# Performance work log

Measured on AMD Instinct MI355X. Metric: run time of the kernel, lower is better.

Reference implementation:

```python
import jax, jax.numpy as jnp
import numpy as np

B, N, C = 4, 16384, 512
HEADS = 16
HEADC = C // HEADS
HIDDEN = int(C * 4.0)


def setup_inputs() -> dict:
    key = jax.random.key(0)
    ks = jax.random.split(key, 8)
    s1 = 1.0 / np.sqrt(C)
    s2 = 1.0 / np.sqrt(HIDDEN)
    return {
        "x": jax.random.normal(ks[0], (B, N, C), jnp.float32),
        "mask_matrix": jnp.zeros((1,), jnp.int32),
        "norm1_w": jnp.ones((C,), jnp.float32),
        "norm1_b": jnp.zeros((C,), jnp.float32),
        "kln_w": jnp.ones((HEADS, 1, HEADC), jnp.float32),
        "kln_b": jnp.zeros((HEADS, 1, HEADC), jnp.float32),
        "vln_w": jnp.ones((HEADS, 1, HEADC), jnp.float32),
        "vln_b": jnp.zeros((HEADS, 1, HEADC), jnp.float32),
        "norm2_w": jnp.ones((C,), jnp.float32),
        "norm2_b": jnp.zeros((C,), jnp.float32),
        "fc1_w": jax.random.uniform(ks[1], (HIDDEN, C), jnp.float32, -s1, s1),
        "fc1_b": jax.random.uniform(ks[2], (HIDDEN,), jnp.float32, -s1, s1),
        "fc2_w": jax.random.uniform(ks[3], (C, HIDDEN), jnp.float32, -s2, s2),
        "fc2_b": jax.random.uniform(ks[4], (C,), jnp.float32, -s2, s2),
    }


def _ln(t, w, b, eps=1e-5):
    # standard nn.LayerNorm: biased variance, eps inside sqrt
    mean = t.mean(-1, keepdims=True)
    var = ((t - mean) ** 2).mean(-1, keepdims=True)
    return w * (t - mean) / jnp.sqrt(var + eps) + b


def _ln_std(t, w, b, eps=1e-5):
    # custom LayerNorm: unbiased std (torch.std), eps added to std
    d = t.shape[-1]
    mean = t.mean(-1, keepdims=True)
    var = ((t - mean) ** 2).sum(-1, keepdims=True) / (d - 1)
    return w * ((t - mean) / (jnp.sqrt(var) + eps)) + b


def reference(x, mask_matrix, norm1_w, norm1_b, kln_w, kln_b, vln_w, vln_b,
              norm2_w, norm2_b, fc1_w, fc1_b, fc2_w, fc2_b):
    b, n, c = x.shape
    shortcut = x
    h = _ln(x, norm1_w, norm1_b)
    # simple_attn (softmax-free linear attention)
    qkv = h.reshape(b, n, HEADS, HEADC).transpose(0, 2, 1, 3)  # [B,H,N,D]
    q = qkv
    k = _ln_std(qkv, kln_w, kln_b)
    v = _ln_std(qkv, vln_w, vln_b)
    kv = jnp.einsum('bhnd,bhne->bhde', k, v) / n        # [B,H,D,D]
    attn = jnp.einsum('bhnd,bhde->bhne', q, kv)          # [B,H,N,D]
    attn = attn.transpose(0, 2, 1, 3).reshape(b, n, c)
    h = attn + h                                          # residual inside simple_attn (bias = x post-norm1)
    x = shortcut + h
    # MLP branch
    m = _ln(x, norm2_w, norm2_b)
    m = jax.nn.gelu(m @ fc1_w.T + fc1_b, approximate=False)
    m = m @ fc2_w.T + fc2_b
    return x + m
```

## Files before the change

kernel.cpp:

```cpp
#include <hip/hip_runtime.h>
#include <cstdint>

#define BB 4
#define NN 16384
#define CC 512
#define HH 16
#define DD 32
#define HID 2048
#define MTOT (BB * NN)

typedef __bf16 bf16_t;
typedef __bf16 bf16x8 __attribute__((ext_vector_type(8)));
typedef __bf16 bf16x4 __attribute__((ext_vector_type(4)));
typedef float  f32x4  __attribute__((ext_vector_type(4)));
typedef float  f32x16 __attribute__((ext_vector_type(16)));

__device__ __forceinline__ void gload_lds16(const void* g, void* l) {
  auto gp = reinterpret_cast<const __attribute__((address_space(1))) char*>(
      reinterpret_cast<uintptr_t>(g));
  auto lp = reinterpret_cast<__attribute__((address_space(3))) char*>(
      reinterpret_cast<uintptr_t>(l));
  __builtin_amdgcn_global_load_lds(gp, lp, 16, 0, 0);
}

__global__ __launch_bounds__(256) void cvt_bf16_kernel(const float* __restrict__ src,
                                                       bf16_t* __restrict__ dst) {
  const long i = ((long)blockIdx.x * 256 + threadIdx.x) * 4;
  const f32x4 v = *(const f32x4*)(src + i);
  bf16x4 o;
  o[0] = (bf16_t)v[0]; o[1] = (bf16_t)v[1]; o[2] = (bf16_t)v[2]; o[3] = (bf16_t)v[3];
  *(bf16x4*)(dst + i) = o;
}

__global__ __launch_bounds__(256) void norm1_kernel(const float* __restrict__ x,
                                                    const float* __restrict__ w,
                                                    const float* __restrict__ bvec,
                                                    bf16_t* __restrict__ h) {
  const int wv = threadIdx.x >> 6, l = threadIdx.x & 63;
  const long tok = (long)blockIdx.x * 4 + wv;
  const int c0 = l * 8;
  const f32x4 a = *(const f32x4*)(x + tok * CC + c0);
  const f32x4 b = *(const f32x4*)(x + tok * CC + c0 + 4);
  float v[8];
#pragma unroll
  for (int i = 0; i < 4; ++i) { v[i] = a[i]; v[4 + i] = b[i]; }
  float s = 0.f, s2 = 0.f;
#pragma unroll
  for (int i = 0; i < 8; ++i) { s += v[i]; s2 += v[i] * v[i]; }
  for (int off = 32; off; off >>= 1) { s += __shfl_xor(s, off); s2 += __shfl_xor(s2, off); }
  const float mean = s * (1.f / CC);
  const float var  = fmaxf(s2 * (1.f / CC) - mean * mean, 0.f);
  const float rstd = rsqrtf(var + 1e-5f);
  const f32x4 w0 = *(const f32x4*)(w + c0), w1 = *(const f32x4*)(w + c0 + 4);
  const f32x4 b0 = *(const f32x4*)(bvec + c0), b1 = *(const f32x4*)(bvec + c0 + 4);
  bf16x8 o;
#pragma unroll
  for (int i = 0; i < 4; ++i) {
    o[i]     = (bf16_t)(w0[i] * (v[i] - mean) * rstd + b0[i]);
    o[4 + i] = (bf16_t)(w1[i] * (v[4 + i] - mean) * rstd + b1[i]);
  }
  *(bf16x8*)(h + tok * CC + c0) = o;
}

__global__ __launch_bounds__(256) void kv_partial_kernel(const bf16_t* __restrict__ h,
                                                         const float* __restrict__ klw,
                                                         const float* __restrict__ klb,
                                                         const float* __restrict__ vlw,
                                                         const float* __restrict__ vlb,
                                                         float* __restrict__ kvp) {
  __shared__ bf16_t kb[256 * 32];
  __shared__ bf16_t vb[256 * 32];
  __shared__ float scratch[192 * 16];
  const int tid = threadIdx.x;
  const int bh = blockIdx.x >> 6, chunk = blockIdx.x & 63;
  const int head = bh & 15;
  const int b = bh >> 4;
  const long tok0 = ((long)b << 14) + chunk * 256;
  const bf16_t* src = h + (tok0 + tid) * (long)CC + head * DD;
  float hv[32];
  {
    float s = 0.f, s2 = 0.f;
#pragma unroll
    for (int c = 0; c < 4; ++c) {
      const bf16x8 r = *(const bf16x8*)(src + c * 8);
#pragma unroll
      for (int j = 0; j < 8; ++j) {
        hv[c * 8 + j] = (float)r[j]; s += hv[c * 8 + j]; s2 += hv[c * 8 + j] * hv[c * 8 + j];
      }
    }
    const float mean = s * (1.f / 32.f);
    const float varu = fmaxf((s2 - 32.f * mean * mean) * (1.f / 31.f), 0.f);
    const float inv = 1.f / (sqrtf(varu) + 1e-5f);
    const int sx = (tid >> 1) & 3;
#pragma unroll
    for (int c = 0; c < 4; ++c) {
      bf16x8 kc, vc;
#pragma unroll
      for (int j = 0; j < 8; ++j) {
        const int d = c * 8 + j;
        const float t = (hv[d] - mean) * inv;
        kc[j] = (bf16_t)(klw[head * DD + d] * t + klb[head * DD + d]);
        vc[j] = (bf16_t)(vlw[head * DD + d] * t + vlb[head * DD + d]);
      }
      *(bf16x8*)((char*)kb + tid * 64 + ((c ^ sx) * 16)) = kc;
      *(bf16x8*)((char*)vb + tid * 64 + ((c ^ sx) * 16)) = vc;
    }
  }
  __syncthreads();
  const int g = tid >> 6, l = tid & 63;
  const int d0 = (l >> 3) * 4, e0 = (l & 7) * 4;
  const int ck = (l >> 3) >> 1, hk = (l >> 3) & 1;
  const int ce = (l & 7) >> 1, he = l & 1;
  float a[4][4] = {};
  for (int t = g; t < 256; t += 4) {
    const int tx = (t >> 1) & 3;
    const bf16x4 kq = *(const bf16x4*)((const char*)kb + t * 64 + ((ck ^ tx) * 16) + hk * 8);
    const bf16x4 vq = *(const bf16x4*)((const char*)vb + t * 64 + ((ce ^ tx) * 16) + he * 8);
    float kf[4], vf[4];
#pragma unroll
    for (int i2 = 0; i2 < 4; ++i2) { kf[i2] = (float)kq[i2]; vf[i2] = (float)vq[i2]; }
#pragma unroll
    for (int i2 = 0; i2 < 4; ++i2)
#pragma unroll
      for (int j2 = 0; j2 < 4; ++j2) a[i2][j2] += kf[i2] * vf[j2];
  }
  __syncthreads();
  if (g) {
#pragma unroll
    for (int i2 = 0; i2 < 4; ++i2)
#pragma unroll
      for (int j2 = 0; j2 < 4; ++j2)
        scratch[((g - 1) * 64 + l) * 16 + i2 * 4 + j2] = a[i2][j2];
  }
  __syncthreads();
  if (!g) {
#pragma unroll
    for (int gg = 0; gg < 3; ++gg)
#pragma unroll
      for (int i2 = 0; i2 < 4; ++i2)
#pragma unroll
        for (int j2 = 0; j2 < 4; ++j2)
          a[i2][j2] += scratch[(gg * 64 + l) * 16 + i2 * 4 + j2];
    float* dst = kvp + ((long)(bh * 64 + chunk) << 10);
#pragma unroll
    for (int i2 = 0; i2 < 4; ++i2) {
      f32x4 st;
      st[0] = a[i2][0]; st[1] = a[i2][1]; st[2] = a[i2][2]; st[3] = a[i2][3];
      *(f32x4*)&dst[(d0 + i2) * 32 + e0] = st;
    }
  }
}

__global__ __launch_bounds__(256) void kv_reduce_kernel(const float* __restrict__ kvp,
                                                        bf16_t* __restrict__ kvT) {
  const int bh = blockIdx.x;
  const int i4 = threadIdx.x * 4;
  const int d = i4 >> 5, e0 = i4 & 31;
  float s[4] = {};
  const float* p = kvp + ((long)bh << 16) + i4;
  for (int ch = 0; ch < 64; ++ch) {
    const f32x4 t = *(const f32x4*)(p + (ch << 10));
    s[0] += t[0]; s[1] += t[1]; s[2] += t[2]; s[3] += t[3];
  }
  const float sc = 1.f / (float)NN;
  bf16_t* q = kvT + ((long)bh << 10);
#pragma unroll
  for (int j = 0; j < 4; ++j) q[(e0 + j) * 32 + d] = (bf16_t)(s[j] * sc);
}

#define ASTRIDE 520
__global__ __launch_bounds__(256) void attn_fused_kernel(const float* __restrict__ x,
                                                         const bf16_t* __restrict__ h,
                                                         const bf16_t* __restrict__ kvTg,
                                                         const float* __restrict__ n2w,
                                                         const float* __restrict__ n2b,
                                                         bf16_t* __restrict__ x2b,
                                                         bf16_t* __restrict__ mout) {
  __shared__ bf16_t attn_s[32 * ASTRIDE];
  const int tid = threadIdx.x;
  const int wv = tid >> 6, lane = tid & 63;
  const int lr = lane & 15, kg = lane >> 4;
  const long tok0 = (long)blockIdx.x * 32;
  const int b = (int)(tok0 >> 14);
  const bf16_t* kvsrc = kvTg + ((long)b << 14);

  {
    const int tt = wv & 1, hh = wv >> 1;
    const bf16_t* arow = h + (tok0 + tt * 16 + lr) * (long)CC + kg * 8;
    const f32x4 zero = {};
#pragma unroll
    for (int hi = 0; hi < 8; ++hi) {
      const int hd = hh * 8 + hi;
      const bf16_t* kvh = kvsrc + (hd << 10) + kg * 8;
      const bf16x8 af = *(const bf16x8*)(arow + hd * DD);
      const bf16x8 b0 = *(const bf16x8*)(kvh + lr * 32);
      const bf16x8 b1 = *(const bf16x8*)(kvh + (16 + lr) * 32);
      const f32x4 a0 = __builtin_amdgcn_mfma_f32_16x16x32_bf16(af, b0, zero, 0, 0, 0);
      const f32x4 a1 = __builtin_amdgcn_mfma_f32_16x16x32_bf16(af, b1, zero, 0, 0, 0);
      const int rbase = tt * 16 + kg * 4;
#pragma unroll
      for (int rg = 0; rg < 4; ++rg) {
        attn_s[(rbase + rg) * ASTRIDE + hd * 32 + lr]      = (bf16_t)a0[rg];
        attn_s[(rbase + rg) * ASTRIDE + hd * 32 + 16 + lr] = (bf16_t)a1[rg];
      }
    }
  }

  const int c0 = lane * 8;
  const f32x4 w0 = *(const f32x4*)(n2w + c0), w1 = *(const f32x4*)(n2w + c0 + 4);
  const f32x4 bb0 = *(const f32x4*)(n2b + c0), bb1 = *(const f32x4*)(n2b + c0 + 4);

  const long tokp = tok0 + wv * 8;
  f32x4 xa = *(const f32x4*)(x + tokp * CC + c0);
  f32x4 xb = *(const f32x4*)(x + tokp * CC + c0 + 4);
  bf16x8 hv = *(const bf16x8*)(h + tokp * CC + c0);
  __syncthreads();

#pragma unroll
  for (int it = 0; it < 8; ++it) {
    const int tl = wv * 8 + it;
    const long tok = tok0 + tl;
    f32x4 xa1, xb1;
    bf16x8 hv1;
    if (it < 7) {
      xa1 = *(const f32x4*)(x + (tok + 1) * CC + c0);
      xb1 = *(const f32x4*)(x + (tok + 1) * CC + c0 + 4);
      hv1 = *(const bf16x8*)(h + (tok + 1) * CC + c0);
    }
    const bf16x8 av = *(const bf16x8*)&attn_s[tl * ASTRIDE + c0];
    float x2[8];
#pragma unroll
    for (int i = 0; i < 4; ++i) {
      x2[i]     = xa[i] + (float)hv[i]     + (float)av[i];
      x2[4 + i] = xb[i] + (float)hv[4 + i] + (float)av[4 + i];
    }
    float s = 0.f, s2 = 0.f;
#pragma unroll
    for (int i = 0; i < 8; ++i) { s += x2[i]; s2 += x2[i] * x2[i]; }
    for (int off = 32; off; off >>= 1) { s += __shfl_xor(s, off); s2 += __shfl_xor(s2, off); }
    const float mean = s * (1.f / CC);
    const float var  = fmaxf(s2 * (1.f / CC) - mean * mean, 0.f);
    const float rstd = rsqrtf(var + 1e-5f);
    bf16x8 ox, om;
#pragma unroll
    for (int i = 0; i < 4; ++i) {
      ox[i]     = (bf16_t)x2[i];
      ox[4 + i] = (bf16_t)x2[4 + i];
      om[i]     = (bf16_t)(w0[i] * (x2[i] - mean) * rstd + bb0[i]);
      om[4 + i] = (bf16_t)(w1[i] * (x2[4 + i] - mean) * rstd + bb1[i]);
    }
    *(bf16x8*)(x2b + tok * CC + c0) = ox;
    *(bf16x8*)(mout + tok * CC + c0) = om;
    xa = xa1; xb = xb1; hv = hv1;
  }
}

template <int K, int NOUT, int BN, bool GELU>
__global__ __launch_bounds__(512, 2) void gemm8p_kernel(const bf16_t* __restrict__ A,
                                                        const bf16_t* __restrict__ Bw,
                                                        const float* __restrict__ bias,
                                                        bf16_t* __restrict__ outb,
                                                        float* __restrict__ outf,
                                                        const bf16_t* __restrict__ x2b) {
  constexpr int NTILE = NOUT / BN;
  constexpr int NT = K / 64;
  constexpr int NI = NT / 2;
  constexpr int WNSPAN = BN / 4;
  constexpr int NF2 = WNSPAN / 32;
  constexpr int BLOADS = BN / 128;
  constexpr int ABYT = 32768;
  constexpr int BBYT = BN * 128;
  constexpr int BUFB = ABYT + BBYT;
  constexpr int KSB = BN * 64;

  __shared__ char lds[2 * BUFB];

  const int tid = threadIdx.x;
  const int wid = tid >> 6, lane = tid & 63;
  const int wm = wid >> 2, wn = wid & 3;
  const int l31 = lane & 31, kg5 = lane >> 5;

  int bid = blockIdx.x;
  const int qq = gridDim.x >> 3;
  bid = (bid & 7) * qq + (bid >> 3);
  const long row0 = (long)(bid / NTILE) * 256;
  const long col0 = (long)(bid % NTILE) * BN;

  const int srow = tid >> 2;
  const int ssw = (((srow >> 1) & 3) ^ ((srow >> 3) & 3));
  const int sce = (((tid & 3) ^ ssw) << 3);
  const bf16_t* pA = A + (row0 + srow) * (long)K + sce;
  const bf16_t* pB = Bw + (col0 + srow) * (long)K + sce;
  char* ldsp = (char*)lds;

  auto SA = [&](int buf, int ks, int kt) {
    char* d_ = ldsp + buf * BUFB + ks * 16384 + tid * 16;
    const bf16_t* g_ = pA + (long)kt * 64 + ks * 32;
    gload_lds16(g_, d_);
    gload_lds16(g_ + 128L * K, d_ + 8192);
  };
  auto SB = [&](int buf, int ks, int kt) {
    char* d_ = ldsp + buf * BUFB + ABYT + ks * KSB + tid * 16;
    const bf16_t* g_ = pB + (long)kt * 64 + ks * 32;
    gload_lds16(g_, d_);
    if constexpr (BLOADS == 2) gload_lds16(g_ + 128L * K, d_ + 8192);
  };

  f32x16 acc[4][NF2] = {};
  bf16x8 af[4], bf[NF2];

  const int swz = ((l31 >> 1) & 3) ^ ((l31 >> 3) & 3);
  const int cb0 = (((0 << 1) | kg5) ^ swz) << 4;
  const int cb1 = (((1 << 1) | kg5) ^ swz) << 4;
  const char* aR = ldsp + (wm * 128 + l31) * 64;
  const char* bR = ldsp + ABYT + (wn * WNSPAN + l31) * 64;

  auto RD = [&](int buf, int ks, int k16) {
    const int cb = k16 ? cb1 : cb0;
    const char* a_ = aR + buf * BUFB + ks * 16384 + cb;
    const char* b_ = bR + buf * BUFB + ks * KSB + cb;
#pragma unroll
    for (int mf = 0; mf < 4; ++mf) af[mf] = *(const bf16x8*)(a_ + mf * 2048);
#pragma unroll
    for (int nf = 0; nf < NF2; ++nf) bf[nf] = *(const bf16x8*)(b_ + nf * 2048);
  };
  auto MM = [&]() {
    __builtin_amdgcn_s_setprio(1);
#pragma unroll
    for (int mf = 0; mf < 4; ++mf)
#pragma unroll
      for (int nf = 0; nf < NF2; ++nf)
        acc[mf][nf] =
            __builtin_amdgcn_mfma_f32_32x32x16_bf16(af[mf], bf[nf], acc[mf][nf], 0, 0, 0);
    __builtin_amdgcn_s_setprio(0);
  };
  auto W2U = [&]() {
    if constexpr (BLOADS == 2) asm volatile("s_waitcnt vmcnt(8)" ::: "memory");
    else                       asm volatile("s_waitcnt vmcnt(6)" ::: "memory");
  };
  auto W1U = [&]() {
    if constexpr (BLOADS == 2) asm volatile("s_waitcnt vmcnt(4)" ::: "memory");
    else                       asm volatile("s_waitcnt vmcnt(3)" ::: "memory");
  };
#define BARX() __builtin_amdgcn_s_barrier()
#define LGKM0() asm volatile("s_waitcnt lgkmcnt(0)" ::: "memory")
#define W0U() asm volatile("s_waitcnt vmcnt(0)" ::: "memory")

  SA(0, 0, 0); SB(0, 0, 0);
  SA(0, 1, 0); SB(0, 1, 0);
  SA(1, 0, 1); SB(1, 0, 1);
  W2U();
  BARX();

  for (int i = 0; i < NI; ++i) {
    const int t1 = 2 * i + 1, tA = 2 * i + 2, tB = 2 * i + 3;
    RD(0, 0, 0); SA(1, 1, t1);
    BARX(); LGKM0(); MM(); BARX();
    RD(0, 0, 1); SB(1, 1, t1);
    BARX(); LGKM0(); MM(); W2U(); BARX();
    RD(0, 1, 0); if (tA < NT) SA(0, 0, tA);
    BARX(); LGKM0(); MM(); BARX();
    RD(0, 1, 1); if (tA < NT) SB(0, 0, tA);
    BARX(); LGKM0(); MM();
    if (tA < NT) W2U(); else W1U();
    BARX();
    RD(1, 0, 0); if (tA < NT) SA(0, 1, tA);
    BARX(); LGKM0(); MM(); BARX();
    RD(1, 0, 1); if (tA < NT) SB(0, 1, tA);
    BARX(); LGKM0(); MM();
    if (tA < NT) W2U(); else W0U();
    BARX();
    RD(1, 1, 0); if (tB < NT) SA(1, 0, tB);
    BARX(); LGKM0(); MM(); BARX();
    RD(1, 1, 1); if (tB < NT) SB(1, 0, tB);
    BARX(); LGKM0(); MM();
    if (tB < NT) W2U();
    BARX();
  }
#undef BARX
#undef LGKM0
#undef W0U

#pragma unroll
  for (int mf = 0; mf < 4; ++mf) {
#pragma unroll
    for (int nf = 0; nf < NF2; ++nf) {
      const long col = col0 + wn * WNSPAN + nf * 32 + l31;
      const float bs = bias[col];
#pragma unroll
      for (int r = 0; r < 16; ++r) {
        const long row = row0 + wm * 128 + mf * 32 + (r & 3) + 8 * (r >> 2) + 4 * kg5;
        const float v = acc[mf][nf][r] + bs;
        if constexpr (GELU) {
          const float u = 0.7978845608028654f * (v + 0.044715f * v * v * v);
          const float gv = v / (1.f + __expf(-2.f * u));
          outb[row * NOUT + col] = (bf16_t)gv;
        } else {
          outf[row * NOUT + col] = (float)x2b[row * NOUT + col] + v;
        }
      }
    }
  }
}

extern "C" void kernel_launch(void* const* d_in, const int* in_sizes, int n_in,
                              void* d_out, int out_size, void* d_ws, size_t ws_size,
                              hipStream_t stream) {
  const float* x   = (const float*)d_in[0];
  const float* n1w = (const float*)d_in[2];
  const float* n1b = (const float*)d_in[3];
  const float* klw = (const float*)d_in[4];
  const float* klb = (const float*)d_in[5];
  const float* vlw = (const float*)d_in[6];
  const float* vlb = (const float*)d_in[7];
  const float* n2w = (const float*)d_in[8];
  const float* n2b = (const float*)d_in[9];
  const float* w1f = (const float*)d_in[10];
  const float* b1  = (const float*)d_in[11];
  const float* w2f = (const float*)d_in[12];
  const float* b2  = (const float*)d_in[13];
  float* out = (float*)d_out;

  int nch;
  if (ws_size >= 360000000ULL) nch = 2;
  else                         nch = 4;
  const long mch = MTOT / nch;

  char* ws = (char*)d_ws;
  size_t off = 0;
  bf16_t* h   = (bf16_t*)(ws + off); off += (size_t)MTOT * CC * 2;
  bf16_t* mb  = (bf16_t*)(ws + off); off += (size_t)MTOT * CC * 2;
  bf16_t* x2b = (bf16_t*)(ws + off); off += (size_t)MTOT * CC * 2;
  bf16_t* act = (bf16_t*)(ws + off); off += (size_t)mch * HID * 2;
  bf16_t* w1  = (bf16_t*)(ws + off); off += (size_t)HID * CC * 2;
  bf16_t* w2  = (bf16_t*)(ws + off); off += (size_t)HID * CC * 2;
  float*  kvp = (float*)(ws + off);  off += (size_t)BB * HH * 64 * 1024 * 4;
  bf16_t* kvT = (bf16_t*)(ws + off);

  cvt_bf16_kernel<<<1024, 256, 0, stream>>>(w1f, w1);
  cvt_bf16_kernel<<<1024, 256, 0, stream>>>(w2f, w2);
  norm1_kernel<<<MTOT / 4, 256, 0, stream>>>(x, n1w, n1b, h);
  kv_partial_kernel<<<BB * HH * 64, 256, 0, stream>>>(h, klw, klb, vlw, vlb, kvp);
  kv_reduce_kernel<<<BB * HH, 256, 0, stream>>>(kvp, kvT);
  attn_fused_kernel<<<MTOT / 32, 256, 0, stream>>>(x, h, kvT, n2w, n2b, x2b, mb);
  for (int ch = 0; ch < nch; ++ch) {
    gemm8p_kernel<CC, HID, 256, true>
        <<<(int)((mch / 256) * (HID / 256)), 512, 0, stream>>>(
        mb + (size_t)ch * mch * CC, w1, b1, act, nullptr, nullptr);
    if (mch >= 32768) {
      gemm8p_kernel<HID, CC, 256, false>
          <<<(int)((mch / 256) * (CC / 256)), 512, 0, stream>>>(
          act, w2, b2, nullptr, out + (size_t)ch * mch * CC,
          x2b + (size_t)ch * mch * CC);
    } else {
      gemm8p_kernel<HID, CC, 128, false>
          <<<(int)((mch / 256) * (CC / 128)), 512, 0, stream>>>(
          act, w2, b2, nullptr, out + (size_t)ch * mch * CC,
          x2b + (size_t)ch * mch * CC);
    }
  }
}
```

Baseline: 573.4 us.

## Software-pipeline MLP GEMMs by co-launching fc1 of next chunk with fc2 of previous

```diff
diff --git a/kernel.cpp b/kernel.cpp
--- a/kernel.cpp
+++ b/kernel.cpp
@@ -209,24 +209,33 @@
   const int c0 = lane * 8;
   const f32x4 w0 = *(const f32x4*)(n2w + c0), w1 = *(const f32x4*)(n2w + c0 + 4);
   const f32x4 bb0 = *(const f32x4*)(n2b + c0), bb1 = *(const f32x4*)(n2b + c0 + 4);
-
-  const long tokp = tok0 + wv * 8;
-  f32x4 xa = *(const f32x4*)(x + tokp * CC + c0);
-  f32x4 xb = *(const f32x4*)(x + tokp * CC + c0 + 4);
-  bf16x8 hv = *(const bf16x8*)(h + tokp * CC + c0);
+  const long tokb = tok0 + wv * 8;
+
+  f32x4 xaA[4], xbA[4];
+  bf16x8 hvA[4];
+#pragma unroll
+  for (int it = 0; it < 4; ++it) {
+    xaA[it] = *(const f32x4*)(x + (tokb + it) * CC + c0);
+    xbA[it] = *(const f32x4*)(x + (tokb + it) * CC + c0 + 4);
+    hvA[it] = *(const bf16x8*)(h + (tokb + it) * CC + c0);
+  }
   __syncthreads();
+  f32x4 xaB[4], xbB[4];
+  bf16x8 hvB[4];
+#pragma unroll
+  for (int it = 0; it < 4; ++it) {
+    xaB[it] = *(const f32x4*)(x + (tokb + 4 + it) * CC + c0);
+    xbB[it] = *(const f32x4*)(x + (tokb + 4 + it) * CC + c0 + 4);
+    hvB[it] = *(const bf16x8*)(h + (tokb + 4 + it) * CC + c0);
+  }
 
 #pragma unroll
   for (int it = 0; it < 8; ++it) {
+    const f32x4 xa = (it < 4) ? xaA[it] : xaB[it - 4];
+    const f32x4 xb = (it < 4) ? xbA[it] : xbB[it - 4];
+    const bf16x8 hv = (it < 4) ? hvA[it] : hvB[it - 4];
     const int tl = wv * 8 + it;
     const long tok = tok0 + tl;
-    f32x4 xa1, xb1;
-    bf16x8 hv1;
-    if (it < 7) {
-      xa1 = *(const f32x4*)(x + (tok + 1) * CC + c0);
-      xb1 = *(const f32x4*)(x + (tok + 1) * CC + c0 + 4);
-      hv1 = *(const bf16x8*)(h + (tok + 1) * CC + c0);
-    }
     const bf16x8 av = *(const bf16x8*)&attn_s[tl * ASTRIDE + c0];
     float x2[8];
 #pragma unroll
@@ -251,23 +260,18 @@
     }
     *(bf16x8*)(x2b + tok * CC + c0) = ox;
     *(bf16x8*)(mout + tok * CC + c0) = om;
-    xa = xa1; xb = xb1; hv = hv1;
-  }
-}
-
-template <int K, int NOUT, int BN, bool GELU>
-__global__ __launch_bounds__(512, 2) void gemm8p_kernel(const bf16_t* __restrict__ A,
-                                                        const bf16_t* __restrict__ Bw,
-                                                        const float* __restrict__ bias,
-                                                        bf16_t* __restrict__ outb,
-                                                        float* __restrict__ outf,
-                                                        const bf16_t* __restrict__ x2b) {
-  constexpr int NTILE = NOUT / BN;
-  constexpr int NT = K / 64;
-  constexpr int NI = NT / 2;
-  constexpr int WNSPAN = BN / 4;
-  constexpr int NF2 = WNSPAN / 32;
-  constexpr int BLOADS = BN / 128;
+  }
+}
+
+__global__ __launch_bounds__(512, 2) void gemm_dual_kernel(
+    const bf16_t* __restrict__ A1, const bf16_t* __restrict__ B1w,
+    const float* __restrict__ bias1, bf16_t* __restrict__ out1b,
+    const bf16_t* __restrict__ A2, const bf16_t* __restrict__ B2w,
+    const float* __restrict__ bias2, float* __restrict__ out2f,
+    const bf16_t* __restrict__ x2b, int g1blocks) {
+  constexpr int BN = 256;
+  constexpr int WNSPAN = 64;
+  constexpr int NF2 = 2;
   constexpr int ABYT = 32768;
   constexpr int BBYT = BN * 128;
   constexpr int BUFB = ABYT + BBYT;
@@ -280,8 +284,19 @@
   const int wm = wid >> 2, wn = wid & 3;
   const int l31 = lane & 31, kg5 = lane >> 5;
 
-  int bid = blockIdx.x;
-  const int qq = gridDim.x >> 3;
+  const bool role1 = ((int)blockIdx.x < g1blocks);
+  const int rblocks = role1 ? g1blocks : ((int)gridDim.x - g1blocks);
+  int bid = role1 ? (int)blockIdx.x : ((int)blockIdx.x - g1blocks);
+  const int K     = role1 ? CC : HID;
+  const long NOUT = role1 ? HID : CC;
+  const int NTILE = role1 ? (HID / BN) : (CC / BN);
+  const int NT    = K / 64;
+  const int NI    = NT / 2;
+  const bf16_t* A    = role1 ? A1 : A2;
+  const bf16_t* Bw   = role1 ? B1w : B2w;
+  const float*  bias = role1 ? bias1 : bias2;
+
+  const int qq = rblocks >> 3;
   bid = (bid & 7) * qq + (bid >> 3);
   const long row0 = (long)(bid / NTILE) * 256;
   const long col0 = (long)(bid % NTILE) * BN;
@@ -303,7 +318,7 @@
     char* d_ = ldsp + buf * BUFB + ABYT + ks * KSB + tid * 16;
     const bf16_t* g_ = pB + (long)kt * 64 + ks * 32;
     gload_lds16(g_, d_);
-    if constexpr (BLOADS == 2) gload_lds16(g_ + 128L * K, d_ + 8192);
+    gload_lds16(g_ + 128L * K, d_ + 8192);
   };
 
   f32x16 acc[4][NF2] = {};
@@ -334,14 +349,8 @@
             __builtin_amdgcn_mfma_f32_32x32x16_bf16(af[mf], bf[nf], acc[mf][nf], 0, 0, 0);
     __builtin_amdgcn_s_setprio(0);
   };
-  auto W2U = [&]() {
-    if constexpr (BLOADS == 2) asm volatile("s_waitcnt vmcnt(8)" ::: "memory");
-    else                       asm volatile("s_waitcnt vmcnt(6)" ::: "memory");
-  };
-  auto W1U = [&]() {
-    if constexpr (BLOADS == 2) asm volatile("s_waitcnt vmcnt(4)" ::: "memory");
-    else                       asm volatile("s_waitcnt vmcnt(3)" ::: "memory");
-  };
+#define W2U() asm volatile("s_waitcnt vmcnt(8)" ::: "memory")
+#define W1U() asm volatile("s_waitcnt vmcnt(4)" ::: "memory")
 #define BARX() __builtin_amdgcn_s_barrier()
 #define LGKM0() asm volatile("s_waitcnt lgkmcnt(0)" ::: "memory")
 #define W0U() asm volatile("s_waitcnt vmcnt(0)" ::: "memory")
@@ -377,6 +386,8 @@
     if (tB < NT) W2U();
     BARX();
   }
+#undef W2U
+#undef W1U
 #undef BARX
 #undef LGKM0
 #undef W0U
@@ -391,12 +402,12 @@
       for (int r = 0; r < 16; ++r) {
         const long row = row0 + wm * 128 + mf * 32 + (r & 3) + 8 * (r >> 2) + 4 * kg5;
         const float v = acc[mf][nf][r] + bs;
-        if constexpr (GELU) {
+        if (role1) {
           const float u = 0.7978845608028654f * (v + 0.044715f * v * v * v);
           const float gv = v / (1.f + __expf(-2.f * u));
-          outb[row * NOUT + col] = (bf16_t)gv;
+          out1b[row * NOUT + col] = (bf16_t)gv;
         } else {
-          outf[row * NOUT + col] = (float)x2b[row * NOUT + col] + v;
+          out2f[row * NOUT + col] = (float)x2b[row * NOUT + col] + v;
         }
       }
     }
@@ -421,21 +432,26 @@
   const float* b2  = (const float*)d_in[13];
   float* out = (float*)d_out;
 
-  int nch;
-  if (ws_size >= 360000000ULL) nch = 2;
-  else                         nch = 4;
+  int nch; bool dual;
+  if (ws_size >= 470000000ULL)      { nch = 2; dual = true;  }
+  else if (ws_size >= 357000000ULL) { nch = 4; dual = true;  }
+  else if (ws_size >= 290000000ULL) { nch = 8; dual = true;  }
+  else                              { nch = 8; dual = false; }
   const long mch = MTOT / nch;
 
   char* ws = (char*)d_ws;
   size_t off = 0;
-  bf16_t* h   = (bf16_t*)(ws + off); off += (size_t)MTOT * CC * 2;
-  bf16_t* mb  = (bf16_t*)(ws + off); off += (size_t)MTOT * CC * 2;
-  bf16_t* x2b = (bf16_t*)(ws + off); off += (size_t)MTOT * CC * 2;
-  bf16_t* act = (bf16_t*)(ws + off); off += (size_t)mch * HID * 2;
+  bf16_t* h    = (bf16_t*)(ws + off); off += (size_t)MTOT * CC * 2;
+  bf16_t* mb   = (bf16_t*)(ws + off); off += (size_t)MTOT * CC * 2;
+  bf16_t* x2b  = (bf16_t*)(ws + off); off += (size_t)MTOT * CC * 2;
+  bf16_t* act0 = (bf16_t*)(ws + off); off += (size_t)mch * HID * 2;
+  bf16_t* act1 = act0;
+  if (dual) { act1 = (bf16_t*)(ws + off); off += (size_t)mch * HID * 2; }
   bf16_t* w1  = (bf16_t*)(ws + off); off += (size_t)HID * CC * 2;
   bf16_t* w2  = (bf16_t*)(ws + off); off += (size_t)HID * CC * 2;
   float*  kvp = (float*)(ws + off);  off += (size_t)BB * HH * 64 * 1024 * 4;
   bf16_t* kvT = (bf16_t*)(ws + off);
+  bf16_t* acts[2] = {act0, act1};
 
   cvt_bf16_kernel<<<1024, 256, 0, stream>>>(w1f, w1);
   cvt_bf16_kernel<<<1024, 256, 0, stream>>>(w2f, w2);
@@ -443,20 +459,33 @@
   kv_partial_kernel<<<BB * HH * 64, 256, 0, stream>>>(h, klw, klb, vlw, vlb, kvp);
   kv_reduce_kernel<<<BB * HH, 256, 0, stream>>>(kvp, kvT);
   attn_fused_kernel<<<MTOT / 32, 256, 0, stream>>>(x, h, kvT, n2w, n2b, x2b, mb);
-  for (int ch = 0; ch < nch; ++ch) {
-    gemm8p_kernel<CC, HID, 256, true>
-        <<<(int)((mch / 256) * (HID / 256)), 512, 0, stream>>>(
-        mb + (size_t)ch * mch * CC, w1, b1, act, nullptr, nullptr);
-    if (mch >= 32768) {
-      gemm8p_kernel<HID, CC, 256, false>
-          <<<(int)((mch / 256) * (CC / 256)), 512, 0, stream>>>(
-          act, w2, b2, nullptr, out + (size_t)ch * mch * CC,
-          x2b + (size_t)ch * mch * CC);
-    } else {
-      gemm8p_kernel<HID, CC, 128, false>
-          <<<(int)((mch / 256) * (CC / 128)), 512, 0, stream>>>(
-          act, w2, b2, nullptr, out + (size_t)ch * mch * CC,
-          x2b + (size_t)ch * mch * CC);
-    }
-  }
-}
+
+  const int g1grid = (int)((mch / 256) * (HID / 256));
+  const int g2grid = (int)((mch / 256) * (CC / 256));
+
+  if (dual) {
+    gemm_dual_kernel<<<g1grid, 512, 0, stream>>>(
+        mb, w1, b1, acts[0],
+        acts[0], w2, b2, out, x2b, g1grid);
+    for (int i = 1; i < nch; ++i) {
+      gemm_dual_kernel<<<g1grid + g2grid, 512, 0, stream>>>(
+          mb + (size_t)i * mch * CC, w1, b1, acts[i & 1],
+          acts[(i - 1) & 1], w2, b2, out + (size_t)(i - 1) * mch * CC,
+          x2b + (size_t)(i - 1) * mch * CC, g1grid);
+    }
+    gemm_dual_kernel<<<g2grid, 512, 0, stream>>>(
+        mb, w1, b1, acts[0],
+        acts[(nch - 1) & 1], w2, b2, out + (size_t)(nch - 1) * mch * CC,
+        x2b + (size_t)(nch - 1) * mch * CC, 0);
+  } else {
+    for (int i = 0; i < nch; ++i) {
+      gemm_dual_kernel<<<g1grid, 512, 0, stream>>>(
+          mb + (size_t)i * mch * CC, w1, b1, acts[0],
+          acts[0], w2, b2, out, x2b, g1grid);
+      gemm_dual_kernel<<<g2grid, 512, 0, stream>>>(
+          mb, w1, b1, acts[0],
+          acts[0], w2, b2, out + (size_t)i * mch * CC,
+          x2b + (size_t)i * mch * CC, 0);
+    }
+  }
+}
```

New measurement: 677.3 us. 18.1% more time.
